# Kernel tuning notes

Measured on AMD Instinct MI355X. Metric: run time of the kernel, lower is better.

The kernel has to match this reference:

```python
import jax, jax.numpy as jnp
import numpy as np

EPS = 1e-4
MAX_LAPLACE_VAR = 1000.0
MAX_DENSITY = 10000.0
BINS = 256

_LAP_KERNEL = jnp.array([[0., 1., 0.], [1., -4., 1.], [0., 1., 0.]], dtype=jnp.float32)[None, None]  # OIHW [1,1,3,3]


def setup_inputs() -> dict:
    key = jax.random.key(0)
    k1, k2 = jax.random.split(key)
    rgb_img = jax.random.uniform(k1, (32, 3, 512, 512), dtype=jnp.float32)
    depth_img = jax.random.normal(k2, (32, 1, 512, 512), dtype=jnp.float32)
    return {"rgb_img": rgb_img, "depth_img": depth_img}


def _rgb_confidence(rgb_img):
    B, C, H, W = rgb_img.shape
    gray = 0.299 * rgb_img[:, 0] + 0.587 * rgb_img[:, 1] + 0.114 * rgb_img[:, 2]  # [B,H,W]
    gray = gray[:, None]  # [B,1,H,W]
    lap = jax.lax.conv_general_dilated(
        gray, _LAP_KERNEL, window_strides=(1, 1), padding=[(1, 1), (1, 1)],
        dimension_numbers=("NCHW", "OIHW", "NCHW"))
    # torch.var default is unbiased (ddof=1)
    laplace_var = jnp.var(lap, axis=(1, 2, 3), ddof=1)

    # integer-valued pixels 0..255 land exactly in histc bins 0..255 (bins=256, min=0, max=255)
    vals = jnp.clip(gray * 255.0, 0.0, 255.0).astype(jnp.int32)  # [B,1,H,W]
    vals = vals.reshape(B, -1)  # [B, H*W]
    bidx = jnp.broadcast_to(jnp.arange(B)[:, None], vals.shape)
    hist = jnp.zeros((B, BINS), jnp.float32).at[bidx, vals].add(1.0)
    p = hist / jnp.sum(hist, axis=1, keepdims=True)
    entropy = -jnp.sum(p * jnp.log2(p + EPS), axis=1)

    clarity_score = laplace_var / (MAX_LAPLACE_VAR + EPS)
    uniformity_score = 1.0 / (entropy + EPS)
    return (0.5 * (clarity_score + uniformity_score))[:, None]  # [B,1]


def _depth_confidence(depth_img):
    C = depth_img.shape[1]
    depth_map = depth_img[:, 2] if C == 3 else depth_img[:, 0]  # [B,H,W]
    mask = (depth_map > 0).astype(jnp.float32)
    density = jnp.mean(mask, axis=(1, 2))

    # vectorized masked std (unbiased, ddof=1), matching torch.std over valid pixels
    n = jnp.sum(mask, axis=(1, 2))  # [B]
    mean = jnp.sum(depth_map * mask, axis=(1, 2)) / jnp.maximum(n, 1.0)
    sq = jnp.sum(mask * (depth_map - mean[:, None, None]) ** 2, axis=(1, 2))
    var = sq / jnp.maximum(n - 1.0, 1.0)
    std = jnp.sqrt(jnp.maximum(var, 0.0))
    noise_level = jnp.where(n > 0, std, 1.0)

    density_score = density / (MAX_DENSITY + EPS)
    noise_score = 1.0 / (noise_level + EPS)
    return (0.5 * (density_score + noise_score))[:, None]  # [B,1]


def reference(rgb_img, depth_img):
    rgb_conf = _rgb_confidence(rgb_img)
    depth_conf = _depth_confidence(depth_img)
    denom = rgb_conf + depth_conf + EPS
    w_r = rgb_conf / denom
    w_d = depth_conf / denom
    return (w_r, w_d)
```

## Files before the change

kernel.cpp:

```cpp
#include <hip/hip_runtime.h>

#define IMG_H 512
#define IMG_W 512
#define HW (IMG_H * IMG_W)
#define NB 32
#define STRIPS 32
#define RPW 4

#define ACC_DOUBLES 160
#define HIST_U32 (NB * 256)
#define WS_BYTES (ACC_DOUBLES * 8 + HIST_U32 * 4)

struct Row6 { float4 a0, a1, b0, b1, c0, c1; };

__device__ inline Row6 load_row(const float* __restrict__ rp, int r, int c0) {
    Row6 x;
    if ((unsigned)r < IMG_H) {
        const size_t o = (size_t)r * IMG_W + c0;
        x.a0 = *(const float4*)(rp + o);
        x.a1 = *(const float4*)(rp + o + 4);
        x.b0 = *(const float4*)(rp + HW + o);
        x.b1 = *(const float4*)(rp + HW + o + 4);
        x.c0 = *(const float4*)(rp + 2 * HW + o);
        x.c1 = *(const float4*)(rp + 2 * HW + o + 4);
    } else {
        const float4 z = {0.f, 0.f, 0.f, 0.f};
        x.a0 = x.a1 = x.b0 = x.b1 = x.c0 = x.c1 = z;
    }
    return x;
}

__device__ inline void to_gray(const Row6& x, float g[8]) {
    g[0] = 0.299f * x.a0.x + 0.587f * x.b0.x + 0.114f * x.c0.x;
    g[1] = 0.299f * x.a0.y + 0.587f * x.b0.y + 0.114f * x.c0.y;
    g[2] = 0.299f * x.a0.z + 0.587f * x.b0.z + 0.114f * x.c0.z;
    g[3] = 0.299f * x.a0.w + 0.587f * x.b0.w + 0.114f * x.c0.w;
    g[4] = 0.299f * x.a1.x + 0.587f * x.b1.x + 0.114f * x.c1.x;
    g[5] = 0.299f * x.a1.y + 0.587f * x.b1.y + 0.114f * x.c1.y;
    g[6] = 0.299f * x.a1.z + 0.587f * x.b1.z + 0.114f * x.c1.z;
    g[7] = 0.299f * x.a1.w + 0.587f * x.b1.w + 0.114f * x.c1.w;
}

__global__ __launch_bounds__(256, 2) void fused_kernel(
    const float* __restrict__ rgb, const float* __restrict__ depth,
    double* __restrict__ acc, unsigned int* __restrict__ hist)
{
    __shared__ unsigned int lh[4][256];
    __shared__ double red[4][5];

    const int t = threadIdx.x;
    const int b = blockIdx.y;
    const int s = blockIdx.x;
    const int lane = t & 63;
    const int w = t >> 6;

    #pragma unroll
    for (int i = 0; i < 4; ++i) lh[i][t] = 0u;
    __syncthreads();

    const float* rp = rgb + (size_t)b * 3 * HW;
    const int rb = s * (4 * RPW) + w * RPW;
    const int c0 = lane * 8;

    const float4* dp = (const float4*)(depth + (size_t)b * HW + (size_t)s * (HW / STRIPS));

    Row6 r0 = load_row(rp, rb - 1, c0);
    Row6 r1 = load_row(rp, rb, c0);
    Row6 buf[3];
    float4 dv[3][2];
    buf[0] = load_row(rp, rb + 1, c0); dv[0][0] = dp[0 * 256 + t]; dv[0][1] = dp[1 * 256 + t];
    buf[1] = load_row(rp, rb + 2, c0); dv[1][0] = dp[2 * 256 + t]; dv[1][1] = dp[3 * 256 + t];
    buf[2] = load_row(rp, rb + 3, c0); dv[2][0] = dp[4 * 256 + t]; dv[2][1] = dp[5 * 256 + t];

    float gp[8], gc[8], gn[8];
    to_gray(r0, gp);
    to_gray(r1, gc);

    float s1 = 0.f, s2 = 0.f;
    float dnf = 0.f, dsf = 0.f, dqf = 0.f;

    #pragma unroll
    for (int r = 0; r < RPW; ++r) {
        const int bi = r % 3;
        to_gray(buf[bi], gn);
        const float4 d0 = dv[bi][0];
        const float4 d1 = dv[bi][1];

        if (r < RPW - 3) {
            buf[bi] = load_row(rp, rb + r + 4, c0);
            dv[bi][0] = dp[(2 * r + 6) * 256 + t];
            dv[bi][1] = dp[(2 * r + 7) * 256 + t];
        }

        float lf = __shfl_up(gc[7], 1, 64);
        if (lane == 0) lf = 0.f;
        float rt = __shfl_down(gc[0], 1, 64);
        if (lane == 63) rt = 0.f;

        #pragma unroll
        for (int j = 0; j < 8; ++j) {
            const float left  = (j == 0) ? lf : gc[j - 1];
            const float right = (j == 7) ? rt : gc[j + 1];
            const float lap = gp[j] + gn[j] + left + right - 4.f * gc[j];
            s1 += lap;
            s2 += lap * lap;
            atomicAdd(&lh[w][(int)fminf(fmaxf(gc[j] * 255.f, 0.f), 255.f)], 1u);
        }

        if (d0.x > 0.f) { dnf += 1.f; dsf += d0.x; dqf += d0.x * d0.x; }
        if (d0.y > 0.f) { dnf += 1.f; dsf += d0.y; dqf += d0.y * d0.y; }
        if (d0.z > 0.f) { dnf += 1.f; dsf += d0.z; dqf += d0.z * d0.z; }
        if (d0.w > 0.f) { dnf += 1.f; dsf += d0.w; dqf += d0.w * d0.w; }
        if (d1.x > 0.f) { dnf += 1.f; dsf += d1.x; dqf += d1.x * d1.x; }
        if (d1.y > 0.f) { dnf += 1.f; dsf += d1.y; dqf += d1.y * d1.y; }
        if (d1.z > 0.f) { dnf += 1.f; dsf += d1.z; dqf += d1.z * d1.z; }
        if (d1.w > 0.f) { dnf += 1.f; dsf += d1.w; dqf += d1.w * d1.w; }

        #pragma unroll
        for (int j = 0; j < 8; ++j) { gp[j] = gc[j]; gc[j] = gn[j]; }
    }

    double z0 = (double)s1, z1 = (double)s2, z2 = (double)dnf, z3 = (double)dsf, z4 = (double)dqf;
    for (int off = 32; off > 0; off >>= 1) {
        z0 += __shfl_down(z0, off, 64);
        z1 += __shfl_down(z1, off, 64);
        z2 += __shfl_down(z2, off, 64);
        z3 += __shfl_down(z3, off, 64);
        z4 += __shfl_down(z4, off, 64);
    }
    if (lane == 0) {
        red[w][0] = z0; red[w][1] = z1; red[w][2] = z2; red[w][3] = z3; red[w][4] = z4;
    }
    __syncthreads();

    const unsigned int hsum = lh[0][t] + lh[1][t] + lh[2][t] + lh[3][t];
    atomicAdd(&hist[b * 256 + t], hsum);
    if (t < 5) {
        const double v = red[0][t] + red[1][t] + red[2][t] + red[3][t];
        atomicAdd(&acc[t * 32 + b], v);
    }
}

__global__ __launch_bounds__(256) void final_kernel(
    const double* __restrict__ acc,
    const unsigned int* __restrict__ hist,
    float* __restrict__ out)
{
    __shared__ float part[256];
    const int t = threadIdx.x;
    const int b = t >> 3;
    const int sl = t & 7;
    float e = 0.f;
    #pragma unroll
    for (int i = 0; i < 32; ++i) {
        const float p = (float)hist[b * 256 + sl * 32 + i] * (1.0f / (float)HW);
        e += p * log2f(p + 1e-4f);
    }
    part[t] = e;
    __syncthreads();

    if (t < NB) {
        float es = 0.f;
        #pragma unroll
        for (int i = 0; i < 8; ++i) es += part[t * 8 + i];
        const double entropy = -(double)es;
        const double N = (double)HW;

        const double ls = acc[t], lq = acc[32 + t];
        const double lvar = (lq - ls * ls / N) / (N - 1.0);
        const double clarity = lvar / (1000.0 + 1e-4);
        const double uniformity = 1.0 / (entropy + 1e-4);
        const double rgb_conf = 0.5 * (clarity + uniformity);

        const double n = acc[64 + t], sdep = acc[96 + t], q = acc[128 + t];
        const double mean = sdep / fmax(n, 1.0);
        const double sq = q - 2.0 * mean * sdep + mean * mean * n;
        const double var = sq / fmax(n - 1.0, 1.0);
        const double stdd = sqrt(fmax(var, 0.0));
        const double noise = (n > 0.0) ? stdd : 1.0;
        const double density = n / N;
        const double depth_conf = 0.5 * (density / (10000.0 + 1e-4) + 1.0 / (noise + 1e-4));

        const double denom = rgb_conf + depth_conf + 1e-4;
        out[t]      = (float)(rgb_conf / denom);
        out[NB + t] = (float)(depth_conf / denom);
    }
}

extern "C" void kernel_launch(void* const* d_in, const int* in_sizes, int n_in,
                              void* d_out, int out_size, void* d_ws, size_t ws_size,
                              hipStream_t stream) {
    const float* rgb   = (const float*)d_in[0];
    const float* depth = (const float*)d_in[1];
    float* out = (float*)d_out;

    double* acc = (double*)d_ws;
    unsigned int* hist = (unsigned int*)((char*)d_ws + ACC_DOUBLES * 8);

    hipMemsetAsync(d_ws, 0, WS_BYTES, stream);

    fused_kernel<<<dim3(STRIPS, NB), 256, 0, stream>>>(rgb, depth, acc, hist);
    final_kernel<<<1, 256, 0, stream>>>(acc, hist, out);
}
```

Baseline: 177.6 us.

## Replace global atomics with per-strip partials and drop workspace memset

```diff
diff --git a/kernel.cpp b/kernel.cpp
--- a/kernel.cpp
+++ b/kernel.cpp
@@ -7,9 +7,9 @@
 #define STRIPS 32
 #define RPW 4
 
-#define ACC_DOUBLES 160
-#define HIST_U32 (NB * 256)
-#define WS_BYTES (ACC_DOUBLES * 8 + HIST_U32 * 4)
+#define ACCP_DOUBLES (5 * NB * STRIPS)
+#define HISTP_U32 (NB * STRIPS * 256)
+#define WS_BYTES (ACCP_DOUBLES * 8 + HISTP_U32 * 4)
 
 struct Row6 { float4 a0, a1, b0, b1, c0, c1; };
 
@@ -43,7 +43,7 @@
 
 __global__ __launch_bounds__(256, 2) void fused_kernel(
     const float* __restrict__ rgb, const float* __restrict__ depth,
-    double* __restrict__ acc, unsigned int* __restrict__ hist)
+    double* __restrict__ accp, unsigned int* __restrict__ histp)
 {
     __shared__ unsigned int lh[4][256];
     __shared__ double red[4][5];
@@ -134,45 +134,55 @@
     __syncthreads();
 
     const unsigned int hsum = lh[0][t] + lh[1][t] + lh[2][t] + lh[3][t];
-    atomicAdd(&hist[b * 256 + t], hsum);
+    histp[((size_t)b * STRIPS + s) * 256 + t] = hsum;
     if (t < 5) {
         const double v = red[0][t] + red[1][t] + red[2][t] + red[3][t];
-        atomicAdd(&acc[t * 32 + b], v);
+        accp[((size_t)t * NB + b) * STRIPS + s] = v;
     }
 }
 
 __global__ __launch_bounds__(256) void final_kernel(
-    const double* __restrict__ acc,
-    const unsigned int* __restrict__ hist,
+    const double* __restrict__ accp,
+    const unsigned int* __restrict__ histp,
     float* __restrict__ out)
 {
-    __shared__ float part[256];
+    __shared__ float ent[4];
+    __shared__ double sacc[5];
+
     const int t = threadIdx.x;
-    const int b = t >> 3;
-    const int sl = t & 7;
-    float e = 0.f;
+    const int b = blockIdx.x;
+    const int lane = t & 63;
+    const int w = t >> 6;
+
+    unsigned int hv = 0u;
     #pragma unroll
-    for (int i = 0; i < 32; ++i) {
-        const float p = (float)hist[b * 256 + sl * 32 + i] * (1.0f / (float)HW);
-        e += p * log2f(p + 1e-4f);
-    }
-    part[t] = e;
+    for (int s = 0; s < STRIPS; ++s)
+        hv += histp[((size_t)b * STRIPS + s) * 256 + t];
+
+    const float p = (float)hv * (1.0f / (float)HW);
+    float term = p * log2f(p + 1e-4f);
+    for (int off = 32; off > 0; off >>= 1) term += __shfl_down(term, off, 64);
+    if (lane == 0) ent[w] = term;
+
+    if (t < 160) {
+        const int k = t >> 5, ss = t & 31;
+        double v = accp[((size_t)k * NB + b) * STRIPS + ss];
+        for (int off = 16; off > 0; off >>= 1) v += __shfl_down(v, off, 32);
+        if (ss == 0) sacc[k] = v;
+    }
     __syncthreads();
 
-    if (t < NB) {
-        float es = 0.f;
-        #pragma unroll
-        for (int i = 0; i < 8; ++i) es += part[t * 8 + i];
-        const double entropy = -(double)es;
+    if (t == 0) {
+        const double entropy = -(double)(ent[0] + ent[1] + ent[2] + ent[3]);
         const double N = (double)HW;
 
-        const double ls = acc[t], lq = acc[32 + t];
+        const double ls = sacc[0], lq = sacc[1];
         const double lvar = (lq - ls * ls / N) / (N - 1.0);
         const double clarity = lvar / (1000.0 + 1e-4);
         const double uniformity = 1.0 / (entropy + 1e-4);
         const double rgb_conf = 0.5 * (clarity + uniformity);
 
-        const double n = acc[64 + t], sdep = acc[96 + t], q = acc[128 + t];
+        const double n = sacc[2], sdep = sacc[3], q = sacc[4];
         const double mean = sdep / fmax(n, 1.0);
         const double sq = q - 2.0 * mean * sdep + mean * mean * n;
         const double var = sq / fmax(n - 1.0, 1.0);
@@ -182,8 +192,8 @@
         const double depth_conf = 0.5 * (density / (10000.0 + 1e-4) + 1.0 / (noise + 1e-4));
 
         const double denom = rgb_conf + depth_conf + 1e-4;
-        out[t]      = (float)(rgb_conf / denom);
-        out[NB + t] = (float)(depth_conf / denom);
+        out[b]      = (float)(rgb_conf / denom);
+        out[NB + b] = (float)(depth_conf / denom);
     }
 }
 
@@ -194,11 +204,10 @@
     const float* depth = (const float*)d_in[1];
     float* out = (float*)d_out;
 
-    double* acc = (double*)d_ws;
-    unsigned int* hist = (unsigned int*)((char*)d_ws + ACC_DOUBLES * 8);
-
-    hipMemsetAsync(d_ws, 0, WS_BYTES, stream);
-
-    fused_kernel<<<dim3(STRIPS, NB), 256, 0, stream>>>(rgb, depth, acc, hist);
-    final_kernel<<<1, 256, 0, stream>>>(acc, hist, out);
-}
+    double* accp = (double*)d_ws;
+    unsigned int* histp = (unsigned int*)((char*)d_ws + ACCP_DOUBLES * 8);
+
+
+    fused_kernel<<<dim3(STRIPS, NB), 256, 0, stream>>>(rgb, depth, accp, histp);
+    final_kernel<<<NB, 256, 0, stream>>>(accp, histp, out);
+}
```

Result: no change. 175.4 us (-1.2%).
